# Kernel tuning notes

Measured on AMD Instinct MI355X. Metric: run time of the kernel, lower is better.

The kernel has to match this reference:

```python
import jax, jax.numpy as jnp
import numpy as np

B, L, H, E = 2, 2048, 8, 64
S = L  # self-attention


def setup_inputs() -> dict:
    key = jax.random.key(0)
    k1, k2, k3, k4, k5 = jax.random.split(key, 5)
    return {
        "queries": jax.random.normal(k1, (B, L, H, E), dtype=jnp.float32),
        "keys": jax.random.normal(k2, (B, S, H, E), dtype=jnp.float32),
        "values": jax.random.normal(k3, (B, S, H, E), dtype=jnp.float32),
        "tau": jax.random.uniform(k4, (B, 1), dtype=jnp.float32),
        "delta": jax.random.normal(k5, (B, S), dtype=jnp.float32),
    }


def reference(queries, keys, values, tau, delta):
    # De-stationary attention: scores = (QK^T) * tau + delta, causal mask, softmax, AV
    E_ = queries.shape[-1]
    scale = 1.0 / jnp.sqrt(jnp.float32(E_))
    tau_b = tau[:, None, None, :]      # [B,1,1,1]
    delta_b = delta[:, None, None, :]  # [B,1,1,S]
    scores = jnp.einsum('blhe,bshe->bhls', queries, keys) * tau_b + delta_b  # [B,H,L,S]
    Lq, Sk = scores.shape[-2], scores.shape[-1]
    causal = jnp.triu(jnp.ones((Lq, Sk), dtype=bool), k=1)  # True = masked
    scores = jnp.where(causal[None, None], -jnp.inf, scores)
    A = jax.nn.softmax(scale * scores, axis=-1)
    V = jnp.einsum('bhls,bshd->blhd', A, values)
    return V
```

## Files before the change

kernel.cpp:

```cpp
#include <hip/hip_runtime.h>


typedef _Float16 h8 __attribute__((ext_vector_type(8)));
typedef _Float16 h2 __attribute__((ext_vector_type(2)));
typedef float f32x4 __attribute__((ext_vector_type(4)));

constexpr int Bc = 2, Lc = 2048, Hc = 8, Ec = 64, Sc = 2048;
constexpr int QTL = 128;
constexpr int NQT = Lc / QTL;
constexpr int KT = 64;
constexpr int LDK = 72;
constexpr int NBH = Bc * Hc;
constexpr float SCALE = 0.125f;
constexpr float LOG2E = 1.44269504088896340736f;

__device__ __forceinline__ h2 pk2(float x, float y) {
  return __builtin_bit_cast(h2, __builtin_amdgcn_cvt_pkrtz(x, y));
}
template <int CTRL>
__device__ __forceinline__ float dpp_f(float x) {
  int r = __builtin_amdgcn_update_dpp(0, __builtin_bit_cast(int, x), CTRL, 0xF, 0xF, true);
  return __builtin_bit_cast(float, r);
}
__device__ __forceinline__ float rowmax16(float x) {
  x = fmaxf(x, dpp_f<0xB1>(x));
  x = fmaxf(x, dpp_f<0x4E>(x));
  x = fmaxf(x, dpp_f<0x124>(x));
  x = fmaxf(x, dpp_f<0x128>(x));
  return x;
}

template <int CH_IT, int EPB, int NIT>
__global__ __launch_bounds__(256, 2)
void dsattn_fwd(const float* __restrict__ Qg, const float* __restrict__ Kg,
                const float* __restrict__ Vg, const float* __restrict__ taug,
                const float* __restrict__ deltag, float* __restrict__ Og,
                _Float16* __restrict__ Opart, float* __restrict__ Mpart,
                float* __restrict__ Lpart) {
  __shared__ __align__(16) _Float16 Ks[2][KT * LDK];
  __shared__ __align__(16) _Float16 Vt[2][Ec * LDK];
  __shared__ __align__(16) _Float16 Pb[4][16 * LDK];

  const int tid = threadIdx.x;
  const int wave = tid >> 6, lane = tid & 63;
  const int quad = lane >> 4, l16 = lane & 15;
  const int srow = tid >> 2;
  const int sec = (tid & 3) << 4;
  const int vrp = ((tid >> 3) + 4 * (tid & 7)) & 31;
  const int ve8 = (tid & 7) << 3;
  _Float16* pb = &Pb[wave][0];
  const int lo = l16 & 1;
  const int pbase = (lo ? 32 : 0) + (l16 & ~1);

  h8 onesf;
#pragma unroll
  for (int j = 0; j < 8; ++j) onesf[j] = (_Float16)1.0f;

  for (int wid = (int)blockIdx.x; wid < NIT; wid += (int)gridDim.x) {
    const int bh = wid & (NBH - 1);
    const int e = wid >> 4;
    int qt = NQT - 1, c0 = 0, pre_e = 0;
    {
      int ee = e, acc = 0;
#pragma unroll
      for (int q = NQT - 1; q >= 0; --q) {
        const int n = (2 * q + 1 + CH_IT) / CH_IT;
        if (ee < n) { qt = q; c0 = ee; pre_e = EPB - acc - n; break; }
        ee -= n; acc += n;
      }
    }
    const int ntiles = 2 * qt + 2;
    const int nch = (ntiles + CH_IT - 1) / CH_IT;
    const int ktBeg = c0 * CH_IT;
    const int ktEnd = min(ktBeg + CH_IT - 1, ntiles - 1);
    const int q0 = qt * QTL;
    const int b = bh >> 3, h = bh & 7;
    const float ct = taug[b] * (SCALE * LOG2E);

    h8 qfrag[2][2];
#pragma unroll
    for (int f = 0; f < 2; ++f)
#pragma unroll
      for (int kk = 0; kk < 2; ++kk) {
        const float* qp = Qg + (((size_t)b * Lc + q0 + 32 * wave + 16 * f + l16) * Hc + h) * Ec
                         + quad * 8 + kk * 32;
        const float4* p = (const float4*)qp;
        union { h8 v; h2 c[4]; } u;
        float4 a0 = p[0], a1 = p[1];
        u.c[0] = pk2(a0.x, a0.y); u.c[1] = pk2(a0.z, a0.w);
        u.c[2] = pk2(a1.x, a1.y); u.c[3] = pk2(a1.z, a1.w);
        qfrag[f][kk] = u.v;
      }

    f32x4 Oacc[2][4], Osum[2];
    float mrow[2][4];
#pragma unroll
    for (int f = 0; f < 2; ++f) {
#pragma unroll
      for (int nt = 0; nt < 4; ++nt) Oacc[f][nt] = (f32x4){0.f, 0.f, 0.f, 0.f};
      Osum[f] = (f32x4){0.f, 0.f, 0.f, 0.f};
#pragma unroll
      for (int r = 0; r < 4; ++r) mrow[f][r] = -1e30f;
    }

    float dcur[4];

    __syncthreads();

    {
      const int kb = ktBeg * KT;
      const float* kp = Kg + (((size_t)b * Sc + kb + srow) * Hc + h) * Ec + sec;
      float4 c0v = ((const float4*)kp)[0], c1v = ((const float4*)kp)[1];
      float4 c2v = ((const float4*)kp)[2], c3v = ((const float4*)kp)[3];
      const float* vp0 = Vg + (((size_t)b * Sc + kb + 2 * vrp) * Hc + h) * Ec + ve8;
      const float* vp1 = vp0 + Hc * Ec;
      float4 r00 = ((const float4*)vp0)[0], r01 = ((const float4*)vp0)[1];
      float4 r10 = ((const float4*)vp1)[0], r11 = ((const float4*)vp1)[1];
#pragma unroll
      for (int nt = 0; nt < 4; ++nt)
        dcur[nt] = deltag[(size_t)b * Sc + kb + nt * 16 + l16] * (SCALE * LOG2E);
      union { h8 v; h2 c[4]; } w0, w1;
      w0.c[0] = pk2(c0v.x, c0v.y); w0.c[1] = pk2(c0v.z, c0v.w);
      w0.c[2] = pk2(c1v.x, c1v.y); w0.c[3] = pk2(c1v.z, c1v.w);
      w1.c[0] = pk2(c2v.x, c2v.y); w1.c[1] = pk2(c2v.z, c2v.w);
      w1.c[2] = pk2(c3v.x, c3v.y); w1.c[3] = pk2(c3v.z, c3v.w);
      *(h8*)&Ks[0][srow * LDK + sec] = w0.v;
      *(h8*)&Ks[0][srow * LDK + sec + 8] = w1.v;
      const float e0[8] = {r00.x, r00.y, r00.z, r00.w, r01.x, r01.y, r01.z, r01.w};
      const float e1[8] = {r10.x, r10.y, r10.z, r10.w, r11.x, r11.y, r11.z, r11.w};
#pragma unroll
      for (int j = 0; j < 8; ++j)
        *(h2*)&Vt[0][(ve8 + j) * LDK + 2 * vrp] = pk2(e0[j], e1[j]);
    }

    for (int kt = ktBeg; kt <= ktEnd; ++kt) {
      const int cur = (kt - ktBeg) & 1;
      const bool pf = (kt < ktEnd);
      const int kbase = kt * KT;

      __syncthreads();

      float4 kn0, kn1, kn2, kn3, vn00, vn01, vn10, vn11;
      float dn[4];
      if (pf) {
        const int nb = (kt + 1) * KT;
        const float* kp = Kg + (((size_t)b * Sc + nb + srow) * Hc + h) * Ec + sec;
        kn0 = ((const float4*)kp)[0]; kn1 = ((const float4*)kp)[1];
        kn2 = ((const float4*)kp)[2]; kn3 = ((const float4*)kp)[3];
        const float* vp0 = Vg + (((size_t)b * Sc + nb + 2 * vrp) * Hc + h) * Ec + ve8;
        const float* vp1 = vp0 + Hc * Ec;
        vn00 = ((const float4*)vp0)[0]; vn01 = ((const float4*)vp0)[1];
        vn10 = ((const float4*)vp1)[0]; vn11 = ((const float4*)vp1)[1];
#pragma unroll
        for (int nt = 0; nt < 4; ++nt)
          dn[nt] = deltag[(size_t)b * Sc + nb + nt * 16 + l16];
      }

      const int wtop = q0 + 32 * wave + 31;
      if (kbase <= wtop) {
        f32x4 Sacc[2][4];
#pragma unroll
        for (int f = 0; f < 2; ++f)
#pragma unroll
          for (int nt = 0; nt < 4; ++nt) Sacc[f][nt] = (f32x4){0.f, 0.f, 0.f, 0.f};
#pragma unroll
        for (int kk = 0; kk < 2; ++kk) {
          h8 bf[4];
#pragma unroll
          for (int nt = 0; nt < 4; ++nt)
            bf[nt] = *(const h8*)&Ks[cur][(nt * 16 + l16) * LDK + quad * 8 + kk * 32];
#pragma unroll
          for (int f = 0; f < 2; ++f)
#pragma unroll
            for (int nt = 0; nt < 4; ++nt)
              Sacc[f][nt] = __builtin_amdgcn_mfma_f32_16x16x32_f16(qfrag[f][kk], bf[nt], Sacc[f][nt], 0, 0, 0);
        }

#pragma unroll
        for (int f = 0; f < 2; ++f) {
          const int fr0 = q0 + 32 * wave + 16 * f;
          float sv[4][4];
#pragma unroll
          for (int nt = 0; nt < 4; ++nt)
#pragma unroll
            for (int r = 0; r < 4; ++r)
              sv[nt][r] = Sacc[f][nt][r] * ct + dcur[nt];
          if (kbase + 63 > fr0) {
#pragma unroll
            for (int nt = 0; nt < 4; ++nt) {
              const int key = kbase + nt * 16 + l16;
#pragma unroll
              for (int r = 0; r < 4; ++r)
                if (key > fr0 + quad * 4 + r) sv[nt][r] = -1e30f;
            }
          }
#pragma unroll
          for (int r = 0; r < 4; ++r) {
            float tm = fmaxf(fmaxf(sv[0][r], sv[1][r]), fmaxf(sv[2][r], sv[3][r]));
            tm = rowmax16(tm);
            float mn = fmaxf(mrow[f][r], tm);
            float alpha = __builtin_amdgcn_exp2f(mrow[f][r] - mn);
            mrow[f][r] = mn;
#pragma unroll
            for (int nt = 0; nt < 4; ++nt)
              sv[nt][r] = __builtin_amdgcn_exp2f(sv[nt][r] - mn);
            Osum[f][r] *= alpha;
#pragma unroll
            for (int nt = 0; nt < 4; ++nt) Oacc[f][nt][r] *= alpha;
          }
#pragma unroll
          for (int r = 0; r < 4; ++r) {
            float o0 = dpp_f<0xB1>(sv[0][r]);
            float o1 = dpp_f<0xB1>(sv[1][r]);
            float o2 = dpp_f<0xB1>(sv[2][r]);
            float o3 = dpp_f<0xB1>(sv[3][r]);
            h2 d0 = lo ? pk2(o2, sv[2][r]) : pk2(sv[0][r], o0);
            h2 d1 = lo ? pk2(o3, sv[3][r]) : pk2(sv[1][r], o1);
            _Float16* pp = &pb[((quad << 2) + r) * LDK + pbase];
            *(h2*)pp = d0;
            *(h2*)(pp + 16) = d1;
          }
          asm volatile("s_waitcnt lgkmcnt(0)" ::: "memory");

          h8 af0 = *(const h8*)&pb[l16 * LDK + quad * 8];
          h8 af1 = *(const h8*)&pb[l16 * LDK + quad * 8 + 32];

#pragma unroll
          for (int nt = 0; nt < 4; ++nt) {
            h8 vf0 = *(const h8*)&Vt[cur][(nt * 16 + l16) * LDK + quad * 8];
            Oacc[f][nt] = __builtin_amdgcn_mfma_f32_16x16x32_f16(af0, vf0, Oacc[f][nt], 0, 0, 0);
            h8 vf1 = *(const h8*)&Vt[cur][(nt * 16 + l16) * LDK + quad * 8 + 32];
            Oacc[f][nt] = __builtin_amdgcn_mfma_f32_16x16x32_f16(af1, vf1, Oacc[f][nt], 0, 0, 0);
          }
          Osum[f] = __builtin_amdgcn_mfma_f32_16x16x32_f16(af0, onesf, Osum[f], 0, 0, 0);
          Osum[f] = __builtin_amdgcn_mfma_f32_16x16x32_f16(af1, onesf, Osum[f], 0, 0, 0);
        }
      }

      if (pf) {
        _Float16* ksn = &Ks[cur ^ 1][0];
        _Float16* vtn = &Vt[cur ^ 1][0];
        union { h8 v; h2 c[4]; } w0, w1;
        w0.c[0] = pk2(kn0.x, kn0.y); w0.c[1] = pk2(kn0.z, kn0.w);
        w0.c[2] = pk2(kn1.x, kn1.y); w0.c[3] = pk2(kn1.z, kn1.w);
        w1.c[0] = pk2(kn2.x, kn2.y); w1.c[1] = pk2(kn2.z, kn2.w);
        w1.c[2] = pk2(kn3.x, kn3.y); w1.c[3] = pk2(kn3.z, kn3.w);
        *(h8*)&ksn[srow * LDK + sec] = w0.v;
        *(h8*)&ksn[srow * LDK + sec + 8] = w1.v;
        const float e0[8] = {vn00.x, vn00.y, vn00.z, vn00.w, vn01.x, vn01.y, vn01.z, vn01.w};
        const float e1[8] = {vn10.x, vn10.y, vn10.z, vn10.w, vn11.x, vn11.y, vn11.z, vn11.w};
#pragma unroll
        for (int j = 0; j < 8; ++j)
          *(h2*)&vtn[(ve8 + j) * LDK + 2 * vrp] = pk2(e0[j], e1[j]);
#pragma unroll
        for (int nt = 0; nt < 4; ++nt) dcur[nt] = dn[nt] * (SCALE * LOG2E);
      }
    }

    if (nch == 1) {
#pragma unroll
      for (int f = 0; f < 2; ++f)
#pragma unroll
        for (int r = 0; r < 4; ++r) {
          const int qrow = q0 + 32 * wave + 16 * f + (quad << 2) + r;
          const float inv = 1.0f / Osum[f][r];
          float* op = Og + (((size_t)b * Lc + qrow) * Hc + h) * Ec;
#pragma unroll
          for (int nt = 0; nt < 4; ++nt) op[nt * 16 + l16] = Oacc[f][nt][r] * inv;
        }
    } else {
      const int en = bh * EPB + pre_e + c0;
      _Float16* op = Opart + (size_t)en * (QTL * Ec);
#pragma unroll
      for (int f = 0; f < 2; ++f)
#pragma unroll
        for (int r = 0; r < 4; ++r) {
          const int row = 32 * wave + 16 * f + (quad << 2) + r;
#pragma unroll
          for (int nt = 0; nt < 4; ++nt)
            op[row * Ec + nt * 16 + l16] = (_Float16)Oacc[f][nt][r];
          if (l16 == 0) {
            Mpart[en * QTL + row] = mrow[f][r];
            Lpart[en * QTL + row] = Osum[f][r];
          }
        }
    }
  }
}

template <int CH_IT, int EPB>
__global__ __launch_bounds__(256, 4)
void dsattn_comb(const _Float16* __restrict__ Opart, const float* __restrict__ Mpart,
                 const float* __restrict__ Lpart, float* __restrict__ Og) {
  const int qt = (CH_IT / 2) + ((int)blockIdx.x >> 2);
  const int slab = (int)blockIdx.x & 3;
  const int bh = (int)blockIdx.y;
  const int b = bh >> 3, h = bh & 7;
  const int nch = (2 * qt + 1 + CH_IT) / CH_IT;
  int pre_e = 0;
#pragma unroll
  for (int q = 0; q < NQT; ++q)
    if (q < qt) pre_e += (2 * q + 1 + CH_IT) / CH_IT;
  const int e0 = bh * EPB + pre_e;

  const int row = slab * 32 + ((int)threadIdx.x >> 3);
  const int col = ((int)threadIdx.x & 7) << 3;

  float ms[8];
  float M = -1e30f;
  for (int c = 0; c < nch; ++c) {
    ms[c] = Mpart[(e0 + c) * QTL + row];
    M = fmaxf(M, ms[c]);
  }
  float acc[8];
#pragma unroll
  for (int i = 0; i < 8; ++i) acc[i] = 0.f;
  float l = 0.f;
  for (int c = 0; c < nch; ++c) {
    const float w = __builtin_amdgcn_exp2f(ms[c] - M);
    l += w * Lpart[(e0 + c) * QTL + row];
    h8 v = *(const h8*)(Opart + (size_t)(e0 + c) * (QTL * Ec) + row * Ec + col);
#pragma unroll
    for (int i = 0; i < 8; ++i) acc[i] += w * (float)v[i];
  }
  const float inv = 1.0f / l;
  float* out = Og + (((size_t)b * Lc + qt * QTL + row) * Hc + h) * Ec + col;
  float4 o0, o1;
  o0.x = acc[0] * inv; o0.y = acc[1] * inv; o0.z = acc[2] * inv; o0.w = acc[3] * inv;
  o1.x = acc[4] * inv; o1.y = acc[5] * inv; o1.z = acc[6] * inv; o1.w = acc[7] * inv;
  ((float4*)out)[0] = o0;
  ((float4*)out)[1] = o1;
}

extern "C" void kernel_launch(void* const* d_in, const int* in_sizes, int n_in,
                              void* d_out, int out_size, void* d_ws, size_t ws_size,
                              hipStream_t stream) {
  const float* Q = (const float*)d_in[0];
  const float* K = (const float*)d_in[1];
  const float* V = (const float*)d_in[2];
  const float* tau = (const float*)d_in[3];
  const float* delta = (const float*)d_in[4];
  float* O = (float*)d_out;

  constexpr int CH = 4;
  constexpr int EPB = 72;
  constexpr int TOT_E = Bc * Hc * EPB;
  constexpr int PERS = 768;
  const size_t need = (size_t)TOT_E * QTL * Ec * 2 + 2 * (size_t)TOT_E * QTL * 4;

  if (ws_size >= need) {
    _Float16* Opart = (_Float16*)d_ws;
    float* Mpart = (float*)(Opart + (size_t)TOT_E * QTL * Ec);
    float* Lpart = Mpart + (size_t)TOT_E * QTL;
    dsattn_fwd<CH, EPB, TOT_E><<<dim3(PERS), 256, 0, stream>>>(
        Q, K, V, tau, delta, O, Opart, Mpart, Lpart);
    dim3 g2((NQT - CH / 2) * 4, Bc * Hc);
    dsattn_comb<CH, EPB><<<g2, 256, 0, stream>>>(Opart, Mpart, Lpart, O);
  } else {
    dsattn_fwd<32, NQT, NQT * NBH><<<dim3(NQT * NBH), 256, 0, stream>>>(
        Q, K, V, tau, delta, O, nullptr, nullptr, nullptr);
  }
}
```

Before: 115.8 us.

## Pre-convert K/V to fp16 in a prep kernel and give each wave its own query chunk

```diff
diff --git a/kernel.cpp b/kernel.cpp
--- a/kernel.cpp
+++ b/kernel.cpp
@@ -6,11 +6,10 @@
 typedef float f32x4 __attribute__((ext_vector_type(4)));
 
 constexpr int Bc = 2, Lc = 2048, Hc = 8, Ec = 64, Sc = 2048;
-constexpr int QTL = 128;
-constexpr int NQT = Lc / QTL;
-constexpr int KT = 64;
+constexpr int NBH = 16;
+constexpr int QS = 32;
+constexpr int NQS = Lc / QS;
 constexpr int LDK = 72;
-constexpr int NBH = Bc * Hc;
 constexpr float SCALE = 0.125f;
 constexpr float LOG2E = 1.44269504088896340736f;
 
@@ -29,287 +28,265 @@
   x = fmaxf(x, dpp_f<0x128>(x));
   return x;
 }
-
-template <int CH_IT, int EPB, int NIT>
-__global__ __launch_bounds__(256, 2)
-void dsattn_fwd(const float* __restrict__ Qg, const float* __restrict__ Kg,
-                const float* __restrict__ Vg, const float* __restrict__ taug,
+__device__ __forceinline__ int ntiles_of(int qsub) {
+  return ((qsub * QS + QS - 1) >> 6) + 1;
+}
+
+__global__ __launch_bounds__(256)
+void dsattn_prep(const float* __restrict__ Kg, const float* __restrict__ Vg,
+                 _Float16* __restrict__ Kh, _Float16* __restrict__ Vt) {
+  const int bh = (int)blockIdx.y;
+  const int b = bh >> 3, h = bh & 7;
+  const int s0 = (int)blockIdx.x * 64;
+  const int tid = (int)threadIdx.x;
+  {
+    const int srow = tid >> 2, sec = (tid & 3) << 4;
+    const float* kp = Kg + (((size_t)b * Sc + s0 + srow) * Hc + h) * Ec + sec;
+    float4 c0 = ((const float4*)kp)[0], c1 = ((const float4*)kp)[1];
+    float4 c2 = ((const float4*)kp)[2], c3 = ((const float4*)kp)[3];
+    union { h8 v; h2 c[4]; } w0, w1;
+    w0.c[0] = pk2(c0.x, c0.y); w0.c[1] = pk2(c0.z, c0.w);
+    w0.c[2] = pk2(c1.x, c1.y); w0.c[3] = pk2(c1.z, c1.w);
+    w1.c[0] = pk2(c2.x, c2.y); w1.c[1] = pk2(c2.z, c2.w);
+    w1.c[2] = pk2(c3.x, c3.y); w1.c[3] = pk2(c3.z, c3.w);
+    _Float16* ko = Kh + ((size_t)bh * Sc + s0 + srow) * Ec + sec;
+    *(h8*)ko = w0.v;
+    *(h8*)(ko + 8) = w1.v;
+  }
+  {
+    const int vrp = tid & 31, e8 = (tid >> 5) << 3;
+    const float* vp0 = Vg + (((size_t)b * Sc + s0 + 2 * vrp) * Hc + h) * Ec + e8;
+    const float* vp1 = vp0 + Hc * Ec;
+    float4 r00 = ((const float4*)vp0)[0], r01 = ((const float4*)vp0)[1];
+    float4 r10 = ((const float4*)vp1)[0], r11 = ((const float4*)vp1)[1];
+    const float e0[8] = {r00.x, r00.y, r00.z, r00.w, r01.x, r01.y, r01.z, r01.w};
+    const float e1[8] = {r10.x, r10.y, r10.z, r10.w, r11.x, r11.y, r11.z, r11.w};
+#pragma unroll
+    for (int j = 0; j < 8; ++j)
+      *(h2*)&Vt[((size_t)bh * Ec + e8 + j) * Sc + s0 + 2 * vrp] = pk2(e0[j], e1[j]);
+  }
+}
+
+template <int CH_T, int EPB, int NIT>
+__global__ __launch_bounds__(256)
+void dsattn_fwd(const float* __restrict__ Qg, const _Float16* __restrict__ Kh,
+                const _Float16* __restrict__ Vt, const float* __restrict__ taug,
                 const float* __restrict__ deltag, float* __restrict__ Og,
                 _Float16* __restrict__ Opart, float* __restrict__ Mpart,
                 float* __restrict__ Lpart) {
-  __shared__ __align__(16) _Float16 Ks[2][KT * LDK];
-  __shared__ __align__(16) _Float16 Vt[2][Ec * LDK];
   __shared__ __align__(16) _Float16 Pb[4][16 * LDK];
 
-  const int tid = threadIdx.x;
+  const int tid = (int)threadIdx.x;
   const int wave = tid >> 6, lane = tid & 63;
   const int quad = lane >> 4, l16 = lane & 15;
-  const int srow = tid >> 2;
-  const int sec = (tid & 3) << 4;
-  const int vrp = ((tid >> 3) + 4 * (tid & 7)) & 31;
-  const int ve8 = (tid & 7) << 3;
+
+  const int w = (int)blockIdx.x * 4 + wave;
+  if (w >= NIT) return;
+  const int bh = w & (NBH - 1);
+  const int e = w >> 4;
+
+  int qsub = NQS - 1, c0 = 0;
+  {
+    int ee = e;
+    for (int q = NQS - 1; q >= 0; --q) {
+      const int n = (ntiles_of(q) + CH_T - 1) / CH_T;
+      if (ee < n) { qsub = q; c0 = ee; break; }
+      ee -= n;
+    }
+  }
+  int pre = 0;
+  for (int q = 0; q < qsub; ++q) pre += (ntiles_of(q) + CH_T - 1) / CH_T;
+
+  const int ntiles = ntiles_of(qsub);
+  const int nch = (ntiles + CH_T - 1) / CH_T;
+  const int ktBeg = c0 * CH_T;
+  const int ktEnd = min(ktBeg + CH_T - 1, ntiles - 1);
+  const int q0 = qsub * QS;
+  const int b = bh >> 3, h = bh & 7;
+  const float ct = taug[b] * (SCALE * LOG2E);
+
+  h8 qfrag[2][2];
+#pragma unroll
+  for (int f = 0; f < 2; ++f)
+#pragma unroll
+    for (int kk = 0; kk < 2; ++kk) {
+      const float* qp = Qg + (((size_t)b * Lc + q0 + 16 * f + l16) * Hc + h) * Ec
+                       + quad * 8 + kk * 32;
+      const float4* p = (const float4*)qp;
+      union { h8 v; h2 c[4]; } u;
+      float4 a0 = p[0], a1 = p[1];
+      u.c[0] = pk2(a0.x, a0.y); u.c[1] = pk2(a0.z, a0.w);
+      u.c[2] = pk2(a1.x, a1.y); u.c[3] = pk2(a1.z, a1.w);
+      qfrag[f][kk] = u.v;
+    }
+
+  h8 onesf;
+#pragma unroll
+  for (int j = 0; j < 8; ++j) onesf[j] = (_Float16)1.0f;
+
+  f32x4 Oacc[2][4], Osum[2];
+  float mrow[2][4];
+#pragma unroll
+  for (int f = 0; f < 2; ++f) {
+#pragma unroll
+    for (int nt = 0; nt < 4; ++nt) Oacc[f][nt] = (f32x4){0.f, 0.f, 0.f, 0.f};
+    Osum[f] = (f32x4){0.f, 0.f, 0.f, 0.f};
+#pragma unroll
+    for (int r = 0; r < 4; ++r) mrow[f][r] = -1e30f;
+  }
+
+  const _Float16* kbh = Kh + (size_t)bh * Sc * Ec;
+  const _Float16* vbh = Vt + (size_t)bh * Ec * Sc;
+  const float* dbh = deltag + (size_t)b * Sc;
+
   _Float16* pb = &Pb[wave][0];
   const int lo = l16 & 1;
   const int pbase = (lo ? 32 : 0) + (l16 & ~1);
 
-  h8 onesf;
-#pragma unroll
-  for (int j = 0; j < 8; ++j) onesf[j] = (_Float16)1.0f;
-
-  for (int wid = (int)blockIdx.x; wid < NIT; wid += (int)gridDim.x) {
-    const int bh = wid & (NBH - 1);
-    const int e = wid >> 4;
-    int qt = NQT - 1, c0 = 0, pre_e = 0;
-    {
-      int ee = e, acc = 0;
-#pragma unroll
-      for (int q = NQT - 1; q >= 0; --q) {
-        const int n = (2 * q + 1 + CH_IT) / CH_IT;
-        if (ee < n) { qt = q; c0 = ee; pre_e = EPB - acc - n; break; }
-        ee -= n; acc += n;
-      }
+  for (int kt = ktBeg; kt <= ktEnd; ++kt) {
+    const int kbase = kt * 64;
+
+    h8 kf[4][2];
+#pragma unroll
+    for (int nt = 0; nt < 4; ++nt)
+#pragma unroll
+      for (int kk = 0; kk < 2; ++kk)
+        kf[nt][kk] = *(const h8*)&kbh[(size_t)(kbase + nt * 16 + l16) * Ec
+                                      + quad * 8 + kk * 32];
+    float dcur[4];
+#pragma unroll
+    for (int nt = 0; nt < 4; ++nt)
+      dcur[nt] = dbh[kbase + nt * 16 + l16] * (SCALE * LOG2E);
+
+    f32x4 Sacc[2][4];
+#pragma unroll
+    for (int f = 0; f < 2; ++f)
+#pragma unroll
+      for (int nt = 0; nt < 4; ++nt) Sacc[f][nt] = (f32x4){0.f, 0.f, 0.f, 0.f};
+#pragma unroll
+    for (int kk = 0; kk < 2; ++kk)
+#pragma unroll
+      for (int f = 0; f < 2; ++f)
+#pragma unroll
+        for (int nt = 0; nt < 4; ++nt)
+          Sacc[f][nt] = __builtin_amdgcn_mfma_f32_16x16x32_f16(qfrag[f][kk], kf[nt][kk], Sacc[f][nt], 0, 0, 0);
+
+    h8 vf[4][2];
+#pragma unroll
+    for (int nt = 0; nt < 4; ++nt)
+#pragma unroll
+      for (int kk = 0; kk < 2; ++kk)
+        vf[nt][kk] = *(const h8*)&vbh[(size_t)(nt * 16 + l16) * Sc + kbase
+                                      + quad * 8 + kk * 32];
+
+#pragma unroll
+    for (int f = 0; f < 2; ++f) {
+      const int fr0 = q0 + 16 * f;
+      float sv[4][4];
+#pragma unroll
+      for (int nt = 0; nt < 4; ++nt)
+#pragma unroll
+        for (int r = 0; r < 4; ++r)
+          sv[nt][r] = Sacc[f][nt][r] * ct + dcur[nt];
+      if (kbase + 63 > fr0) {
+#pragma unroll
+        for (int nt = 0; nt < 4; ++nt) {
+          const int key = kbase + nt * 16 + l16;
+#pragma unroll
+          for (int r = 0; r < 4; ++r)
+            if (key > fr0 + quad * 4 + r) sv[nt][r] = -1e30f;
+        }
+      }
+#pragma unroll
+      for (int r = 0; r < 4; ++r) {
+        float tm = fmaxf(fmaxf(sv[0][r], sv[1][r]), fmaxf(sv[2][r], sv[3][r]));
+        tm = rowmax16(tm);
+        float mn = fmaxf(mrow[f][r], tm);
+        float alpha = __builtin_amdgcn_exp2f(mrow[f][r] - mn);
+        mrow[f][r] = mn;
+#pragma unroll
+        for (int nt = 0; nt < 4; ++nt)
+          sv[nt][r] = __builtin_amdgcn_exp2f(sv[nt][r] - mn);
+        Osum[f][r] *= alpha;
+#pragma unroll
+        for (int nt = 0; nt < 4; ++nt) Oacc[f][nt][r] *= alpha;
+      }
+#pragma unroll
+      for (int r = 0; r < 4; ++r) {
+        float o0 = dpp_f<0xB1>(sv[0][r]);
+        float o1 = dpp_f<0xB1>(sv[1][r]);
+        float o2 = dpp_f<0xB1>(sv[2][r]);
+        float o3 = dpp_f<0xB1>(sv[3][r]);
+        h2 d0 = lo ? pk2(o2, sv[2][r]) : pk2(sv[0][r], o0);
+        h2 d1 = lo ? pk2(o3, sv[3][r]) : pk2(sv[1][r], o1);
+        _Float16* pp = &pb[((quad << 2) + r) * LDK + pbase];
+        *(h2*)pp = d0;
+        *(h2*)(pp + 16) = d1;
+      }
+      asm volatile("s_waitcnt lgkmcnt(0)" ::: "memory");
+
+      h8 af0 = *(const h8*)&pb[l16 * LDK + quad * 8];
+      h8 af1 = *(const h8*)&pb[l16 * LDK + quad * 8 + 32];
+
+#pragma unroll
+      for (int nt = 0; nt < 4; ++nt) {
+        Oacc[f][nt] = __builtin_amdgcn_mfma_f32_16x16x32_f16(af0, vf[nt][0], Oacc[f][nt], 0, 0, 0);
+        Oacc[f][nt] = __builtin_amdgcn_mfma_f32_16x16x32_f16(af1, vf[nt][1], Oacc[f][nt], 0, 0, 0);
+      }
+      Osum[f] = __builtin_amdgcn_mfma_f32_16x16x32_f16(af0, onesf, Osum[f], 0, 0, 0);
+      Osum[f] = __builtin_amdgcn_mfma_f32_16x16x32_f16(af1, onesf, Osum[f], 0, 0, 0);
     }
-    const int ntiles = 2 * qt + 2;
-    const int nch = (ntiles + CH_IT - 1) / CH_IT;
-    const int ktBeg = c0 * CH_IT;
-    const int ktEnd = min(ktBeg + CH_IT - 1, ntiles - 1);
-    const int q0 = qt * QTL;
-    const int b = bh >> 3, h = bh & 7;
-    const float ct = taug[b] * (SCALE * LOG2E);
-
-    h8 qfrag[2][2];
+  }
+
+  if (nch == 1) {
 #pragma unroll
     for (int f = 0; f < 2; ++f)
 #pragma unroll
-      for (int kk = 0; kk < 2; ++kk) {
-        const float* qp = Qg + (((size_t)b * Lc + q0 + 32 * wave + 16 * f + l16) * Hc + h) * Ec
-                         + quad * 8 + kk * 32;
-        const float4* p = (const float4*)qp;
-        union { h8 v; h2 c[4]; } u;
-        float4 a0 = p[0], a1 = p[1];
-        u.c[0] = pk2(a0.x, a0.y); u.c[1] = pk2(a0.z, a0.w);
-        u.c[2] = pk2(a1.x, a1.y); u.c[3] = pk2(a1.z, a1.w);
-        qfrag[f][kk] = u.v;
-      }
-
-    f32x4 Oacc[2][4], Osum[2];
-    float mrow[2][4];
-#pragma unroll
-    for (int f = 0; f < 2; ++f) {
-#pragma unroll
-      for (int nt = 0; nt < 4; ++nt) Oacc[f][nt] = (f32x4){0.f, 0.f, 0.f, 0.f};
-      Osum[f] = (f32x4){0.f, 0.f, 0.f, 0.f};
-#pragma unroll
-      for (int r = 0; r < 4; ++r) mrow[f][r] = -1e30f;
-    }
-
-    float dcur[4];
-
-    __syncthreads();
-
-    {
-      const int kb = ktBeg * KT;
-      const float* kp = Kg + (((size_t)b * Sc + kb + srow) * Hc + h) * Ec + sec;
-      float4 c0v = ((const float4*)kp)[0], c1v = ((const float4*)kp)[1];
-      float4 c2v = ((const float4*)kp)[2], c3v = ((const float4*)kp)[3];
-      const float* vp0 = Vg + (((size_t)b * Sc + kb + 2 * vrp) * Hc + h) * Ec + ve8;
-      const float* vp1 = vp0 + Hc * Ec;
-      float4 r00 = ((const float4*)vp0)[0], r01 = ((const float4*)vp0)[1];
-      float4 r10 = ((const float4*)vp1)[0], r11 = ((const float4*)vp1)[1];
-#pragma unroll
-      for (int nt = 0; nt < 4; ++nt)
-        dcur[nt] = deltag[(size_t)b * Sc + kb + nt * 16 + l16] * (SCALE * LOG2E);
-      union { h8 v; h2 c[4]; } w0, w1;
-      w0.c[0] = pk2(c0v.x, c0v.y); w0.c[1] = pk2(c0v.z, c0v.w);
-      w0.c[2] = pk2(c1v.x, c1v.y); w0.c[3] = pk2(c1v.z, c1v.w);
-      w1.c[0] = pk2(c2v.x, c2v.y); w1.c[1] = pk2(c2v.z, c2v.w);
-      w1.c[2] = pk2(c3v.x, c3v.y); w1.c[3] = pk2(c3v.z, c3v.w);
-      *(h8*)&Ks[0][srow * LDK + sec] = w0.v;
-      *(h8*)&Ks[0][srow * LDK + sec + 8] = w1.v;
-      const float e0[8] = {r00.x, r00.y, r00.z, r00.w, r01.x, r01.y, r01.z, r01.w};
-      const float e1[8] = {r10.x, r10.y, r10.z, r10.w, r11.x, r11.y, r11.z, r11.w};
-#pragma unroll
-      for (int j = 0; j < 8; ++j)
-        *(h2*)&Vt[0][(ve8 + j) * LDK + 2 * vrp] = pk2(e0[j], e1[j]);
-    }
-
-    for (int kt = ktBeg; kt <= ktEnd; ++kt) {
-      const int cur = (kt - ktBeg) & 1;
-      const bool pf = (kt < ktEnd);
-      const int kbase = kt * KT;
-
-      __syncthreads();
-
-      float4 kn0, kn1, kn2, kn3, vn00, vn01, vn10, vn11;
-      float dn[4];
-      if (pf) {
-        const int nb = (kt + 1) * KT;
-        const float* kp = Kg + (((size_t)b * Sc + nb + srow) * Hc + h) * Ec + sec;
-        kn0 = ((const float4*)kp)[0]; kn1 = ((const float4*)kp)[1];
-        kn2 = ((const float4*)kp)[2]; kn3 = ((const float4*)kp)[3];
-        const float* vp0 = Vg + (((size_t)b * Sc + nb + 2 * vrp) * Hc + h) * Ec + ve8;
-        const float* vp1 = vp0 + Hc * Ec;
-        vn00 = ((const float4*)vp0)[0]; vn01 = ((const float4*)vp0)[1];
-        vn10 = ((const float4*)vp1)[0]; vn11 = ((const float4*)vp1)[1];
+      for (int r = 0; r < 4; ++r) {
+        const int qrow = q0 + 16 * f + (quad << 2) + r;
+        const float inv = 1.0f / Osum[f][r];
+        float* op = Og + (((size_t)b * Lc + qrow) * Hc + h) * Ec;
+#pragma unroll
+        for (int nt = 0; nt < 4; ++nt) op[nt * 16 + l16] = Oacc[f][nt][r] * inv;
+      }
+  } else {
+    const int ews = bh * EPB + pre + c0;
+    _Float16* op = Opart + (size_t)ews * (QS * Ec);
+#pragma unroll
+    for (int f = 0; f < 2; ++f)
+#pragma unroll
+      for (int r = 0; r < 4; ++r) {
+        const int row = 16 * f + (quad << 2) + r;
 #pragma unroll
         for (int nt = 0; nt < 4; ++nt)
-          dn[nt] = deltag[(size_t)b * Sc + nb + nt * 16 + l16];
-      }
-
-      const int wtop = q0 + 32 * wave + 31;
-      if (kbase <= wtop) {
-        f32x4 Sacc[2][4];
-#pragma unroll
-        for (int f = 0; f < 2; ++f)
-#pragma unroll
-          for (int nt = 0; nt < 4; ++nt) Sacc[f][nt] = (f32x4){0.f, 0.f, 0.f, 0.f};
-#pragma unroll
-        for (int kk = 0; kk < 2; ++kk) {
-          h8 bf[4];
-#pragma unroll
-          for (int nt = 0; nt < 4; ++nt)
-            bf[nt] = *(const h8*)&Ks[cur][(nt * 16 + l16) * LDK + quad * 8 + kk * 32];
-#pragma unroll
-          for (int f = 0; f < 2; ++f)
-#pragma unroll
-            for (int nt = 0; nt < 4; ++nt)
-              Sacc[f][nt] = __builtin_amdgcn_mfma_f32_16x16x32_f16(qfrag[f][kk], bf[nt], Sacc[f][nt], 0, 0, 0);
+          op[row * Ec + nt * 16 + l16] = (_Float16)Oacc[f][nt][r];
+        if (l16 == 0) {
+          Mpart[ews * QS + row] = mrow[f][r];
+          Lpart[ews * QS + row] = Osum[f][r];
         }
-
-#pragma unroll
-        for (int f = 0; f < 2; ++f) {
-          const int fr0 = q0 + 32 * wave + 16 * f;
-          float sv[4][4];
-#pragma unroll
-          for (int nt = 0; nt < 4; ++nt)
-#pragma unroll
-            for (int r = 0; r < 4; ++r)
-              sv[nt][r] = Sacc[f][nt][r] * ct + dcur[nt];
-          if (kbase + 63 > fr0) {
-#pragma unroll
-            for (int nt = 0; nt < 4; ++nt) {
-              const int key = kbase + nt * 16 + l16;
-#pragma unroll
-              for (int r = 0; r < 4; ++r)
-                if (key > fr0 + quad * 4 + r) sv[nt][r] = -1e30f;
-            }
-          }
-#pragma unroll
-          for (int r = 0; r < 4; ++r) {
-            float tm = fmaxf(fmaxf(sv[0][r], sv[1][r]), fmaxf(sv[2][r], sv[3][r]));
-            tm = rowmax16(tm);
-            float mn = fmaxf(mrow[f][r], tm);
-            float alpha = __builtin_amdgcn_exp2f(mrow[f][r] - mn);
-            mrow[f][r] = mn;
-#pragma unroll
-            for (int nt = 0; nt < 4; ++nt)
-              sv[nt][r] = __builtin_amdgcn_exp2f(sv[nt][r] - mn);
-            Osum[f][r] *= alpha;
-#pragma unroll
-            for (int nt = 0; nt < 4; ++nt) Oacc[f][nt][r] *= alpha;
-          }
-#pragma unroll
-          for (int r = 0; r < 4; ++r) {
-            float o0 = dpp_f<0xB1>(sv[0][r]);
-            float o1 = dpp_f<0xB1>(sv[1][r]);
-            float o2 = dpp_f<0xB1>(sv[2][r]);
-            float o3 = dpp_f<0xB1>(sv[3][r]);
-            h2 d0 = lo ? pk2(o2, sv[2][r]) : pk2(sv[0][r], o0);
-            h2 d1 = lo ? pk2(o3, sv[3][r]) : pk2(sv[1][r], o1);
-            _Float16* pp = &pb[((quad << 2) + r) * LDK + pbase];
-            *(h2*)pp = d0;
-            *(h2*)(pp + 16) = d1;
-          }
-          asm volatile("s_waitcnt lgkmcnt(0)" ::: "memory");
-
-          h8 af0 = *(const h8*)&pb[l16 * LDK + quad * 8];
-          h8 af1 = *(const h8*)&pb[l16 * LDK + quad * 8 + 32];
-
-#pragma unroll
-          for (int nt = 0; nt < 4; ++nt) {
-            h8 vf0 = *(const h8*)&Vt[cur][(nt * 16 + l16) * LDK + quad * 8];
-            Oacc[f][nt] = __builtin_amdgcn_mfma_f32_16x16x32_f16(af0, vf0, Oacc[f][nt], 0, 0, 0);
-            h8 vf1 = *(const h8*)&Vt[cur][(nt * 16 + l16) * LDK + quad * 8 + 32];
-            Oacc[f][nt] = __builtin_amdgcn_mfma_f32_16x16x32_f16(af1, vf1, Oacc[f][nt], 0, 0, 0);
-          }
-          Osum[f] = __builtin_amdgcn_mfma_f32_16x16x32_f16(af0, onesf, Osum[f], 0, 0, 0);
-          Osum[f] = __builtin_amdgcn_mfma_f32_16x16x32_f16(af1, onesf, Osum[f], 0, 0, 0);
-        }
-      }
-
-      if (pf) {
-        _Float16* ksn = &Ks[cur ^ 1][0];
-        _Float16* vtn = &Vt[cur ^ 1][0];
-        union { h8 v; h2 c[4]; } w0, w1;
-        w0.c[0] = pk2(kn0.x, kn0.y); w0.c[1] = pk2(kn0.z, kn0.w);
-        w0.c[2] = pk2(kn1.x, kn1.y); w0.c[3] = pk2(kn1.z, kn1.w);
-        w1.c[0] = pk2(kn2.x, kn2.y); w1.c[1] = pk2(kn2.z, kn2.w);
-        w1.c[2] = pk2(kn3.x, kn3.y); w1.c[3] = pk2(kn3.z, kn3.w);
-        *(h8*)&ksn[srow * LDK + sec] = w0.v;
-        *(h8*)&ksn[srow * LDK + sec + 8] = w1.v;
-        const float e0[8] = {vn00.x, vn00.y, vn00.z, vn00.w, vn01.x, vn01.y, vn01.z, vn01.w};
-        const float e1[8] = {vn10.x, vn10.y, vn10.z, vn10.w, vn11.x, vn11.y, vn11.z, vn11.w};
-#pragma unroll
-        for (int j = 0; j < 8; ++j)
-          *(h2*)&vtn[(ve8 + j) * LDK + 2 * vrp] = pk2(e0[j], e1[j]);
-#pragma unroll
-        for (int nt = 0; nt < 4; ++nt) dcur[nt] = dn[nt] * (SCALE * LOG2E);
-      }
-    }
-
-    if (nch == 1) {
-#pragma unroll
-      for (int f = 0; f < 2; ++f)
-#pragma unroll
-        for (int r = 0; r < 4; ++r) {
-          const int qrow = q0 + 32 * wave + 16 * f + (quad << 2) + r;
-          const float inv = 1.0f / Osum[f][r];
-          float* op = Og + (((size_t)b * Lc + qrow) * Hc + h) * Ec;
-#pragma unroll
-          for (int nt = 0; nt < 4; ++nt) op[nt * 16 + l16] = Oacc[f][nt][r] * inv;
-        }
-    } else {
-      const int en = bh * EPB + pre_e + c0;
-      _Float16* op = Opart + (size_t)en * (QTL * Ec);
-#pragma unroll
-      for (int f = 0; f < 2; ++f)
-#pragma unroll
-        for (int r = 0; r < 4; ++r) {
-          const int row = 32 * wave + 16 * f + (quad << 2) + r;
-#pragma unroll
-          for (int nt = 0; nt < 4; ++nt)
-            op[row * Ec + nt * 16 + l16] = (_Float16)Oacc[f][nt][r];
-          if (l16 == 0) {
-            Mpart[en * QTL + row] = mrow[f][r];
-            Lpart[en * QTL + row] = Osum[f][r];
-          }
-        }
-    }
-  }
-}
-
-template <int CH_IT, int EPB>
-__global__ __launch_bounds__(256, 4)
+      }
+  }
+}
+
+template <int CH_T, int EPB>
+__global__ __launch_bounds__(256)
 void dsattn_comb(const _Float16* __restrict__ Opart, const float* __restrict__ Mpart,
                  const float* __restrict__ Lpart, float* __restrict__ Og) {
-  const int qt = (CH_IT / 2) + ((int)blockIdx.x >> 2);
-  const int slab = (int)blockIdx.x & 3;
+  const int qsub = 2 * CH_T + (int)blockIdx.x;
   const int bh = (int)blockIdx.y;
   const int b = bh >> 3, h = bh & 7;
-  const int nch = (2 * qt + 1 + CH_IT) / CH_IT;
-  int pre_e = 0;
-#pragma unroll
-  for (int q = 0; q < NQT; ++q)
-    if (q < qt) pre_e += (2 * q + 1 + CH_IT) / CH_IT;
-  const int e0 = bh * EPB + pre_e;
-
-  const int row = slab * 32 + ((int)threadIdx.x >> 3);
+  const int nch = (ntiles_of(qsub) + CH_T - 1) / CH_T;
+  int pre = 0;
+  for (int q = 0; q < qsub; ++q) pre += (ntiles_of(q) + CH_T - 1) / CH_T;
+  const int e0 = bh * EPB + pre;
+
+  const int row = (int)threadIdx.x >> 3;
   const int col = ((int)threadIdx.x & 7) << 3;
 
   float ms[8];
   float M = -1e30f;
   for (int c = 0; c < nch; ++c) {
-    ms[c] = Mpart[(e0 + c) * QTL + row];
+    ms[c] = Mpart[(e0 + c) * QS + row];
     M = fmaxf(M, ms[c]);
   }
   float acc[8];
@@ -317,14 +294,14 @@
   for (int i = 0; i < 8; ++i) acc[i] = 0.f;
   float l = 0.f;
   for (int c = 0; c < nch; ++c) {
-    const float w = __builtin_amdgcn_exp2f(ms[c] - M);
-    l += w * Lpart[(e0 + c) * QTL + row];
-    h8 v = *(const h8*)(Opart + (size_t)(e0 + c) * (QTL * Ec) + row * Ec + col);
-#pragma unroll
-    for (int i = 0; i < 8; ++i) acc[i] += w * (float)v[i];
+    const float wgt = __builtin_amdgcn_exp2f(ms[c] - M);
+    l += wgt * Lpart[(e0 + c) * QS + row];
+    h8 v = *(const h8*)(Opart + (size_t)(e0 + c) * (QS * Ec) + row * Ec + col);
+#pragma unroll
+    for (int i = 0; i < 8; ++i) acc[i] += wgt * (float)v[i];
   }
   const float inv = 1.0f / l;
-  float* out = Og + (((size_t)b * Lc + qt * QTL + row) * Hc + h) * Ec + col;
+  float* out = Og + (((size_t)b * Lc + qsub * QS + row) * Hc + h) * Ec + col;
   float4 o0, o1;
   o0.x = acc[0] * inv; o0.y = acc[1] * inv; o0.z = acc[2] * inv; o0.w = acc[3] * inv;
   o1.x = acc[4] * inv; o1.y = acc[5] * inv; o1.z = acc[6] * inv; o1.w = acc[7] * inv;
@@ -343,21 +320,27 @@
   float* O = (float*)d_out;
 
   constexpr int CH = 4;
-  constexpr int EPB = 72;
-  constexpr int TOT_E = Bc * Hc * EPB;
-  constexpr int PERS = 768;
-  const size_t need = (size_t)TOT_E * QTL * Ec * 2 + 2 * (size_t)TOT_E * QTL * 4;
-
-  if (ws_size >= need) {
-    _Float16* Opart = (_Float16*)d_ws;
-    float* Mpart = (float*)(Opart + (size_t)TOT_E * QTL * Ec);
-    float* Lpart = Mpart + (size_t)TOT_E * QTL;
-    dsattn_fwd<CH, EPB, TOT_E><<<dim3(PERS), 256, 0, stream>>>(
-        Q, K, V, tau, delta, O, Opart, Mpart, Lpart);
-    dim3 g2((NQT - CH / 2) * 4, Bc * Hc);
-    dsattn_comb<CH, EPB><<<g2, 256, 0, stream>>>(Opart, Mpart, Lpart, O);
+  constexpr int EPB = 288;
+  constexpr int NIT = EPB * NBH;
+  constexpr size_t KVH = (size_t)NBH * Sc * Ec;
+
+  _Float16* Kh = (_Float16*)d_ws;
+  _Float16* Vt = Kh + KVH;
+  _Float16* Opart = Vt + KVH;
+  float* Mpart = (float*)(Opart + (size_t)NIT * QS * Ec);
+  float* Lpart = Mpart + (size_t)NIT * QS;
+  const size_t need_split = 2 * KVH * 2 + (size_t)NIT * QS * Ec * 2
+                          + 2 * (size_t)NIT * QS * 4;
+
+  dsattn_prep<<<dim3(Sc / 64, NBH), 256, 0, stream>>>(K, V, Kh, Vt);
+
+  if (ws_size >= need_split) {
+    dsattn_fwd<CH, EPB, NIT><<<dim3((NIT + 3) / 4), 256, 0, stream>>>(
+        Q, Kh, Vt, tau, delta, O, Opart, Mpart, Lpart);
+    dsattn_comb<CH, EPB><<<dim3(NQS - 2 * CH, NBH), 256, 0, stream>>>(
+        Opart, Mpart, Lpart, O);
   } else {
-    dsattn_fwd<32, NQT, NQT * NBH><<<dim3(NQT * NBH), 256, 0, stream>>>(
-        Q, K, V, tau, delta, O, nullptr, nullptr, nullptr);
-  }
-}
+    dsattn_fwd<32, NQS, NQS * NBH><<<dim3((NQS * NBH + 3) / 4), 256, 0, stream>>>(
+        Q, Kh, Vt, tau, delta, O, nullptr, nullptr, nullptr);
+  }
+}
```

New measurement: 141.7 us. 1.22x slower.

## Prefetch next work item's first K/V tile and Q across persistent loop iterations

Applied to the files above, without the earlier changes.

```diff
diff --git a/kernel.cpp b/kernel.cpp
--- a/kernel.cpp
+++ b/kernel.cpp
@@ -30,7 +30,19 @@
   return x;
 }
 
-template <int CH_IT, int EPB, int NIT>
+template <int CH_IT, int EPB>
+__device__ __forceinline__ void decode_item(int e, int& qt, int& c0, int& pre_e) {
+  qt = NQT - 1; c0 = 0; pre_e = 0;
+  int ee = e, acc = 0;
+#pragma unroll
+  for (int q = NQT - 1; q >= 0; --q) {
+    const int n = (2 * q + 1 + CH_IT) / CH_IT;
+    if (ee < n) { qt = q; c0 = ee; pre_e = EPB - acc - n; break; }
+    ee -= n; acc += n;
+  }
+}
+
+template <int CH_IT, int EPB, int NIT, int GRID>
 __global__ __launch_bounds__(256, 2)
 void dsattn_fwd(const float* __restrict__ Qg, const float* __restrict__ Kg,
                 const float* __restrict__ Vg, const float* __restrict__ taug,
@@ -56,41 +68,68 @@
 #pragma unroll
   for (int j = 0; j < 8; ++j) onesf[j] = (_Float16)1.0f;
 
-  for (int wid = (int)blockIdx.x; wid < NIT; wid += (int)gridDim.x) {
-    const int bh = wid & (NBH - 1);
-    const int e = wid >> 4;
-    int qt = NQT - 1, c0 = 0, pre_e = 0;
-    {
-      int ee = e, acc = 0;
-#pragma unroll
-      for (int q = NQT - 1; q >= 0; --q) {
-        const int n = (2 * q + 1 + CH_IT) / CH_IT;
-        if (ee < n) { qt = q; c0 = ee; pre_e = EPB - acc - n; break; }
-        ee -= n; acc += n;
-      }
+  int wid = (int)blockIdx.x;
+  if (wid >= NIT) return;
+  const int bh = wid & (NBH - 1);
+  const int b = bh >> 3, h = bh & 7;
+  const float ct = taug[b] * (SCALE * LOG2E);
+
+  int qt, c0, pre_e;
+  decode_item<CH_IT, EPB>(wid >> 4, qt, c0, pre_e);
+  int ktBeg = c0 * CH_IT;
+  int ktEnd = min(ktBeg + CH_IT - 1, 2 * qt + 1);
+  int nch = (2 * qt + 1 + CH_IT) / CH_IT;
+  int q0 = qt * QTL;
+
+  h8 qfrag[2][2];
+#pragma unroll
+  for (int f = 0; f < 2; ++f)
+#pragma unroll
+    for (int kk = 0; kk < 2; ++kk) {
+      const float* qp = Qg + (((size_t)b * Lc + q0 + 32 * wave + 16 * f + l16) * Hc + h) * Ec
+                       + quad * 8 + kk * 32;
+      const float4* p = (const float4*)qp;
+      union { h8 v; h2 c[4]; } u;
+      float4 a0 = p[0], a1 = p[1];
+      u.c[0] = pk2(a0.x, a0.y); u.c[1] = pk2(a0.z, a0.w);
+      u.c[2] = pk2(a1.x, a1.y); u.c[3] = pk2(a1.z, a1.w);
+      qfrag[f][kk] = u.v;
     }
-    const int ntiles = 2 * qt + 2;
-    const int nch = (ntiles + CH_IT - 1) / CH_IT;
-    const int ktBeg = c0 * CH_IT;
-    const int ktEnd = min(ktBeg + CH_IT - 1, ntiles - 1);
-    const int q0 = qt * QTL;
-    const int b = bh >> 3, h = bh & 7;
-    const float ct = taug[b] * (SCALE * LOG2E);
-
-    h8 qfrag[2][2];
-#pragma unroll
-    for (int f = 0; f < 2; ++f)
-#pragma unroll
-      for (int kk = 0; kk < 2; ++kk) {
-        const float* qp = Qg + (((size_t)b * Lc + q0 + 32 * wave + 16 * f + l16) * Hc + h) * Ec
-                         + quad * 8 + kk * 32;
-        const float4* p = (const float4*)qp;
-        union { h8 v; h2 c[4]; } u;
-        float4 a0 = p[0], a1 = p[1];
-        u.c[0] = pk2(a0.x, a0.y); u.c[1] = pk2(a0.z, a0.w);
-        u.c[2] = pk2(a1.x, a1.y); u.c[3] = pk2(a1.z, a1.w);
-        qfrag[f][kk] = u.v;
-      }
+
+  float dcur[4];
+  {
+    const int kb = ktBeg * KT;
+    const float* kp = Kg + (((size_t)b * Sc + kb + srow) * Hc + h) * Ec + sec;
+    float4 c0v = ((const float4*)kp)[0], c1v = ((const float4*)kp)[1];
+    float4 c2v = ((const float4*)kp)[2], c3v = ((const float4*)kp)[3];
+    const float* vp0 = Vg + (((size_t)b * Sc + kb + 2 * vrp) * Hc + h) * Ec + ve8;
+    const float* vp1 = vp0 + Hc * Ec;
+    float4 r00 = ((const float4*)vp0)[0], r01 = ((const float4*)vp0)[1];
+    float4 r10 = ((const float4*)vp1)[0], r11 = ((const float4*)vp1)[1];
+#pragma unroll
+    for (int nt = 0; nt < 4; ++nt)
+      dcur[nt] = deltag[(size_t)b * Sc + kb + nt * 16 + l16] * (SCALE * LOG2E);
+    union { h8 v; h2 c[4]; } w0, w1;
+    w0.c[0] = pk2(c0v.x, c0v.y); w0.c[1] = pk2(c0v.z, c0v.w);
+    w0.c[2] = pk2(c1v.x, c1v.y); w0.c[3] = pk2(c1v.z, c1v.w);
+    w1.c[0] = pk2(c2v.x, c2v.y); w1.c[1] = pk2(c2v.z, c2v.w);
+    w1.c[2] = pk2(c3v.x, c3v.y); w1.c[3] = pk2(c3v.z, c3v.w);
+    *(h8*)&Ks[0][srow * LDK + sec] = w0.v;
+    *(h8*)&Ks[0][srow * LDK + sec + 8] = w1.v;
+    const float e0[8] = {r00.x, r00.y, r00.z, r00.w, r01.x, r01.y, r01.z, r01.w};
+    const float e1[8] = {r10.x, r10.y, r10.z, r10.w, r11.x, r11.y, r11.z, r11.w};
+#pragma unroll
+    for (int j = 0; j < 8; ++j)
+      *(h2*)&Vt[0][(ve8 + j) * LDK + 2 * vrp] = pk2(e0[j], e1[j]);
+  }
+
+  int cur = 0;
+  h8 qfn[2][2];
+  int nqt, nc0, npre, nktBeg, nktEnd, nnch, nq0;
+
+  while (true) {
+    const bool has_next = (wid + GRID) < NIT;
+    const int wtop = q0 + 32 * wave + 31;
 
     f32x4 Oacc[2][4], Osum[2];
     float mrow[2][4];
@@ -103,47 +142,40 @@
       for (int r = 0; r < 4; ++r) mrow[f][r] = -1e30f;
     }
 
-    float dcur[4];
-
-    __syncthreads();
-
-    {
-      const int kb = ktBeg * KT;
-      const float* kp = Kg + (((size_t)b * Sc + kb + srow) * Hc + h) * Ec + sec;
-      float4 c0v = ((const float4*)kp)[0], c1v = ((const float4*)kp)[1];
-      float4 c2v = ((const float4*)kp)[2], c3v = ((const float4*)kp)[3];
-      const float* vp0 = Vg + (((size_t)b * Sc + kb + 2 * vrp) * Hc + h) * Ec + ve8;
-      const float* vp1 = vp0 + Hc * Ec;
-      float4 r00 = ((const float4*)vp0)[0], r01 = ((const float4*)vp0)[1];
-      float4 r10 = ((const float4*)vp1)[0], r11 = ((const float4*)vp1)[1];
-#pragma unroll
-      for (int nt = 0; nt < 4; ++nt)
-        dcur[nt] = deltag[(size_t)b * Sc + kb + nt * 16 + l16] * (SCALE * LOG2E);
-      union { h8 v; h2 c[4]; } w0, w1;
-      w0.c[0] = pk2(c0v.x, c0v.y); w0.c[1] = pk2(c0v.z, c0v.w);
-      w0.c[2] = pk2(c1v.x, c1v.y); w0.c[3] = pk2(c1v.z, c1v.w);
-      w1.c[0] = pk2(c2v.x, c2v.y); w1.c[1] = pk2(c2v.z, c2v.w);
-      w1.c[2] = pk2(c3v.x, c3v.y); w1.c[3] = pk2(c3v.z, c3v.w);
-      *(h8*)&Ks[0][srow * LDK + sec] = w0.v;
-      *(h8*)&Ks[0][srow * LDK + sec + 8] = w1.v;
-      const float e0[8] = {r00.x, r00.y, r00.z, r00.w, r01.x, r01.y, r01.z, r01.w};
-      const float e1[8] = {r10.x, r10.y, r10.z, r10.w, r11.x, r11.y, r11.z, r11.w};
-#pragma unroll
-      for (int j = 0; j < 8; ++j)
-        *(h2*)&Vt[0][(ve8 + j) * LDK + 2 * vrp] = pk2(e0[j], e1[j]);
-    }
-
     for (int kt = ktBeg; kt <= ktEnd; ++kt) {
-      const int cur = (kt - ktBeg) & 1;
-      const bool pf = (kt < ktEnd);
+      const bool pf_this = (kt < ktEnd);
+      const bool pf_next = (!pf_this) && has_next;
       const int kbase = kt * KT;
 
       __syncthreads();
 
       float4 kn0, kn1, kn2, kn3, vn00, vn01, vn10, vn11;
       float dn[4];
-      if (pf) {
-        const int nb = (kt + 1) * KT;
+      if (pf_this || pf_next) {
+        int nb;
+        if (pf_this) {
+          nb = (kt + 1) * KT;
+        } else {
+          decode_item<CH_IT, EPB>((wid + GRID) >> 4, nqt, nc0, npre);
+          nktBeg = nc0 * CH_IT;
+          nktEnd = min(nktBeg + CH_IT - 1, 2 * nqt + 1);
+          nnch = (2 * nqt + 1 + CH_IT) / CH_IT;
+          nq0 = nqt * QTL;
+          nb = nktBeg * KT;
+#pragma unroll
+          for (int f = 0; f < 2; ++f)
+#pragma unroll
+            for (int kk = 0; kk < 2; ++kk) {
+              const float* qp = Qg + (((size_t)b * Lc + nq0 + 32 * wave + 16 * f + l16) * Hc + h) * Ec
+                               + quad * 8 + kk * 32;
+              const float4* p = (const float4*)qp;
+              union { h8 v; h2 c[4]; } u;
+              float4 a0 = p[0], a1 = p[1];
+              u.c[0] = pk2(a0.x, a0.y); u.c[1] = pk2(a0.z, a0.w);
+              u.c[2] = pk2(a1.x, a1.y); u.c[3] = pk2(a1.z, a1.w);
+              qfn[f][kk] = u.v;
+            }
+        }
         const float* kp = Kg + (((size_t)b * Sc + nb + srow) * Hc + h) * Ec + sec;
         kn0 = ((const float4*)kp)[0]; kn1 = ((const float4*)kp)[1];
         kn2 = ((const float4*)kp)[2]; kn3 = ((const float4*)kp)[3];
@@ -156,7 +188,6 @@
           dn[nt] = deltag[(size_t)b * Sc + nb + nt * 16 + l16];
       }
 
-      const int wtop = q0 + 32 * wave + 31;
       if (kbase <= wtop) {
         f32x4 Sacc[2][4];
 #pragma unroll
@@ -237,7 +268,7 @@
         }
       }
 
-      if (pf) {
+      if (pf_this || pf_next) {
         _Float16* ksn = &Ks[cur ^ 1][0];
         _Float16* vtn = &Vt[cur ^ 1][0];
         union { h8 v; h2 c[4]; } w0, w1;
@@ -254,6 +285,7 @@
           *(h2*)&vtn[(ve8 + j) * LDK + 2 * vrp] = pk2(e0[j], e1[j]);
 #pragma unroll
         for (int nt = 0; nt < 4; ++nt) dcur[nt] = dn[nt] * (SCALE * LOG2E);
+        cur ^= 1;
       }
     }
 
@@ -285,6 +317,15 @@
           }
         }
     }
+
+    if (!has_next) break;
+    wid += GRID;
+    qt = nqt; c0 = nc0; pre_e = npre;
+    ktBeg = nktBeg; ktEnd = nktEnd; nch = nnch; q0 = nq0;
+#pragma unroll
+    for (int f = 0; f < 2; ++f)
+#pragma unroll
+      for (int kk = 0; kk < 2; ++kk) qfrag[f][kk] = qfn[f][kk];
   }
 }
 
@@ -345,19 +386,19 @@
   constexpr int CH = 4;
   constexpr int EPB = 72;
   constexpr int TOT_E = Bc * Hc * EPB;
-  constexpr int PERS = 768;
+  constexpr int PERS = 576;
   const size_t need = (size_t)TOT_E * QTL * Ec * 2 + 2 * (size_t)TOT_E * QTL * 4;
 
   if (ws_size >= need) {
     _Float16* Opart = (_Float16*)d_ws;
     float* Mpart = (float*)(Opart + (size_t)TOT_E * QTL * Ec);
     float* Lpart = Mpart + (size_t)TOT_E * QTL;
-    dsattn_fwd<CH, EPB, TOT_E><<<dim3(PERS), 256, 0, stream>>>(
+    dsattn_fwd<CH, EPB, TOT_E, PERS><<<dim3(PERS), 256, 0, stream>>>(
         Q, K, V, tau, delta, O, Opart, Mpart, Lpart);
     dim3 g2((NQT - CH / 2) * 4, Bc * Hc);
     dsattn_comb<CH, EPB><<<g2, 256, 0, stream>>>(Opart, Mpart, Lpart, O);
   } else {
-    dsattn_fwd<32, NQT, NQT * NBH><<<dim3(NQT * NBH), 256, 0, stream>>>(
+    dsattn_fwd<32, NQT, NQT * NBH, NQT * NBH><<<dim3(NQT * NBH), 256, 0, stream>>>(
         Q, K, V, tau, delta, O, nullptr, nullptr, nullptr);
   }
 }
```

Measured after the change: 125.0 us. 1.08x slower.
